# Kernel optimization log

Hardware: AMD Instinct MI355X
Metric: run time of the kernel (lower is better)

The kernel has to match this reference:

```python
import jax, jax.numpy as jnp
import numpy as np

N_SRC0, N_DST0 = 200000, 50000
N_DST1 = 10000
D_IN, D_HID = 128, 128


def _sage_mean(h, src, dst, n_dst, W_self, b_self, W_neigh, b_neigh, act):
    # gather messages from src nodes, mean-aggregate per dst node
    msg = h[src]                                             # [E, D]
    agg = jax.ops.segment_sum(msg, dst, num_segments=n_dst)  # [n_dst, D]
    deg = jax.ops.segment_sum(jnp.ones(dst.shape, h.dtype), dst, num_segments=n_dst)
    h_neigh = agg / jnp.maximum(deg, 1.0)[:, None]
    # DGL block convention: dst nodes are the first n_dst src nodes
    rst = h[:n_dst] @ W_self + b_self + h_neigh @ W_neigh + b_neigh
    return jax.nn.relu(rst) if act else rst


def setup_inputs() -> dict:
    key = jax.random.key(0)
    ks = jax.random.split(key, 12)
    s = 1.0 / np.sqrt(D_HID)
    return {
        "features": jax.random.normal(ks[0], (N_SRC0, D_IN), jnp.float32),
        "src0": jax.random.randint(ks[1], (800000,), 0, N_SRC0),
        "dst0": jax.random.randint(ks[2], (800000,), 0, N_DST0),
        "src1": jax.random.randint(ks[3], (160000,), 0, N_DST0),
        "dst1": jax.random.randint(ks[4], (160000,), 0, N_DST1),
        "W_init": jax.random.uniform(ks[5], (D_IN, D_HID), jnp.float32, -s, s),
        "b_init": jax.random.uniform(ks[6], (D_HID,), jnp.float32, -s, s),
        "W_self": jax.random.uniform(ks[7], (D_HID, D_HID), jnp.float32, -s, s),
        "b_self": jax.random.uniform(ks[8], (D_HID,), jnp.float32, -s, s),
        "W_neigh": jax.random.uniform(ks[9], (D_HID, D_HID), jnp.float32, -s, s),
        "b_neigh": jax.random.uniform(ks[10], (D_HID,), jnp.float32, -s, s),
    }


def reference(features, src0, dst0, src1, dst1, W_init, b_init, W_self, b_self, W_neigh, b_neigh):
    # fc_init + activation
    h = jax.nn.relu(features @ W_init + b_init)              # [N_SRC0, D_HID]
    # block 0 (act_flag True), dropout p=0.0 is identity
    h = _sage_mean(h, src0, dst0, N_DST0, W_self, b_self, W_neigh, b_neigh, act=True)
    # block 1 (last block: act_flag False)
    h = _sage_mean(h, src1, dst1, N_DST1, W_self, b_self, W_neigh, b_neigh, act=False)
    return jnp.squeeze(h, axis=1) if h.shape[1] == 1 else h  # h.squeeze(1) no-op for D_HID>1
```

## Files before the change

kernel.cpp:

```cpp
#include <hip/hip_runtime.h>
#include <stdint.h>
#include <stddef.h>


#define DIM 128
constexpr int N_SRC0 = 200000;
constexpr int N_DST0 = 50000;
constexpr int N_DST1 = 10000;
constexpr int E0 = 800000;
constexpr int E1 = 160000;
constexpr int MAXDEG = 64;

constexpr int FC_BLOCKS = 1024;
constexpr int PLACE_BLOCKS = 1024;
constexpr int PREP_BLOCKS = 16;

typedef __attribute__((ext_vector_type(8))) short bf16x8;
typedef __attribute__((ext_vector_type(4))) float f32x4;

__device__ __forceinline__ uint16_t f2bf(float f) {
  union { float f; uint32_t u; } v; v.f = f;
  return (uint16_t)((v.u + 0x7FFFu + ((v.u >> 16) & 1u)) >> 16);
}
__device__ __forceinline__ float bf2f(uint16_t h) {
  union { uint32_t u; float f; } v; v.u = ((uint32_t)h) << 16;
  return v.f;
}

__global__ __launch_bounds__(256, 4) void place_fc_kernel(
    const int* __restrict__ src0, const int* __restrict__ dst0,
    const int* __restrict__ src1, const int* __restrict__ dst1,
    int* __restrict__ cnt0, int* __restrict__ cnt1,
    int* __restrict__ eslot0, int* __restrict__ eslot1,
    const float* __restrict__ feat, const float* __restrict__ W_init,
    const float* __restrict__ bias, uint16_t* __restrict__ hout,
    const float* __restrict__ WS_src, const float* __restrict__ WN_src,
    uint16_t* __restrict__ Wf_out) {
  __shared__ __align__(16) float tile[2][4096];

  if (blockIdx.x >= PLACE_BLOCKS + FC_BLOCKS) {
    int pid = (blockIdx.x - (PLACE_BLOCKS + FC_BLOCKS)) * 256 + threadIdx.x;
#pragma unroll
    for (int u = 0; u < 8; u++) {
      int gid = pid * 8 + u;
      int m = gid >> 14, idx = gid & 16383;
      const float* W = m ? WN_src : WS_src;
      int j = idx & 7, lane = (idx >> 3) & 63, nt = (idx >> 9) & 7, kc = idx >> 12;
      int k = kc * 32 + (lane >> 4) * 8 + j;
      int n = nt * 16 + (lane & 15);
      Wf_out[gid] = f2bf(W[k * DIM + n]);
    }
    return;
  }

  if ((blockIdx.x & 1) == 0) {
    int pb = blockIdx.x >> 1;
    int part = pb & 7;
    int bpp  = PLACE_BLOCKS >> 3;
    int bidx = pb >> 3;
    const int4* s04 = (const int4*)src0;
    const int4* d04 = (const int4*)dst0;
    const int4* s14 = (const int4*)src1;
    const int4* d14 = (const int4*)dst1;

    int lo = part * (N_DST0 / 8), hi = lo + (N_DST0 / 8);
    for (int i = bidx * 256 + threadIdx.x; i < E0 / 4; i += bpp * 256) {
      int4 d = d04[i]; int4 s = s04[i];
      if (d.x >= lo && d.x < hi) { int p = atomicAdd(&cnt0[d.x], 1); if (p < MAXDEG) eslot0[(size_t)d.x * MAXDEG + p] = s.x; }
      if (d.y >= lo && d.y < hi) { int p = atomicAdd(&cnt0[d.y], 1); if (p < MAXDEG) eslot0[(size_t)d.y * MAXDEG + p] = s.y; }
      if (d.z >= lo && d.z < hi) { int p = atomicAdd(&cnt0[d.z], 1); if (p < MAXDEG) eslot0[(size_t)d.z * MAXDEG + p] = s.z; }
      if (d.w >= lo && d.w < hi) { int p = atomicAdd(&cnt0[d.w], 1); if (p < MAXDEG) eslot0[(size_t)d.w * MAXDEG + p] = s.w; }
    }
    int lo1 = part * (N_DST1 / 8), hi1 = lo1 + (N_DST1 / 8);
    for (int i = bidx * 256 + threadIdx.x; i < E1 / 4; i += bpp * 256) {
      int4 d = d14[i]; int4 s = s14[i];
      if (d.x >= lo1 && d.x < hi1) { int p = atomicAdd(&cnt1[d.x], 1); if (p < MAXDEG) eslot1[(size_t)d.x * MAXDEG + p] = s.x; }
      if (d.y >= lo1 && d.y < hi1) { int p = atomicAdd(&cnt1[d.y], 1); if (p < MAXDEG) eslot1[(size_t)d.y * MAXDEG + p] = s.y; }
      if (d.z >= lo1 && d.z < hi1) { int p = atomicAdd(&cnt1[d.z], 1); if (p < MAXDEG) eslot1[(size_t)d.z * MAXDEG + p] = s.z; }
      if (d.w >= lo1 && d.w < hi1) { int p = atomicAdd(&cnt1[d.w], 1); if (p < MAXDEG) eslot1[(size_t)d.w * MAXDEG + p] = s.w; }
    }
    return;
  }

  const int tid = threadIdx.x;
  const int w = tid >> 6, lane = tid & 63;
  const int q = lane >> 4, m16 = lane & 15;
  const int sl = w >> 1, nh = w & 1;

  {
    uint16_t* wtmp = (uint16_t*)tile;
    for (int u = 0; u < 8; u++) {
      int c = u * 256 + tid;
      int lane_c = c & 63;
      int nt = (c >> 6) & 7;
      int kc = c >> 9;
      int k0 = kc * 32 + (lane_c >> 4) * 8;
      int n  = nt * 16 + (lane_c & 15);
      bf16x8 frag;
#pragma unroll
      for (int j = 0; j < 8; j++)
        frag[j] = (short)f2bf(W_init[(size_t)(k0 + j) * DIM + n]);
      *(bf16x8*)&wtmp[(size_t)c * 8] = frag;
    }
  }
  __syncthreads();

  bf16x8 wv[4][4];
  {
    const uint16_t* wtmp = (const uint16_t*)tile;
#pragma unroll
    for (int kc = 0; kc < 4; kc++)
#pragma unroll
      for (int jj = 0; jj < 4; jj++)
        wv[kc][jj] = *(const bf16x8*)&wtmp[((kc * 8 + nh * 4 + jj) * 64 + lane) * 8];
  }
  __syncthreads();

  float bv[4];
#pragma unroll
  for (int j = 0; j < 4; j++) bv[j] = bias[(nh * 4 + j) * 16 + m16];

  const int ntiles = N_SRC0 / 32;

  const int lrow0 = w * 8 + (lane >> 5);
  auto stage = [&](int t, int buf) {
#pragma unroll
    for (int i = 0; i < 4; i++) {
      int row = lrow0 + i * 2;
      int g = (lane & 31) ^ (row & 7);
      const float* gs = feat + (size_t)t * 4096 + row * 128 + g * 4;
      float* ld = &tile[buf][w * 1024 + i * 256];
      __builtin_amdgcn_global_load_lds(
          (const __attribute__((address_space(1))) uint32_t*)gs,
          (__attribute__((address_space(3))) uint32_t*)ld,
          16, 0, 0);
    }
  };

  int t = blockIdx.x >> 1;
  int cur = 0;
  if (t < ntiles) stage(t, 0);

  const int trow = sl * 16 + m16;
  const int sw = trow & 7;

  while (t < ntiles) {
    int tn = t + FC_BLOCKS;
    if (tn < ntiles) {
      stage(tn, cur ^ 1);
      asm volatile("s_waitcnt vmcnt(4)" ::: "memory");
    } else {
      asm volatile("s_waitcnt vmcnt(0)" ::: "memory");
    }
    __builtin_amdgcn_s_barrier();
    __builtin_amdgcn_sched_barrier(0);

    f32x4 acc[4];
#pragma unroll
    for (int j = 0; j < 4; j++) acc[j] = (f32x4){0.f, 0.f, 0.f, 0.f};

    const char* rb = (const char*)&tile[cur][0] + trow * 512;
#pragma unroll
    for (int kc = 0; kc < 4; kc++) {
      int g0 = kc * 8 + q * 2;
      float4 x0 = *(const float4*)(rb + ((g0    ) ^ sw) * 16);
      float4 x1 = *(const float4*)(rb + ((g0 + 1) ^ sw) * 16);
      bf16x8 a;
      a[0] = (short)f2bf(x0.x); a[1] = (short)f2bf(x0.y);
      a[2] = (short)f2bf(x0.z); a[3] = (short)f2bf(x0.w);
      a[4] = (short)f2bf(x1.x); a[5] = (short)f2bf(x1.y);
      a[6] = (short)f2bf(x1.z); a[7] = (short)f2bf(x1.w);
#pragma unroll
      for (int j = 0; j < 4; j++)
        acc[j] = __builtin_amdgcn_mfma_f32_16x16x32_bf16(a, wv[kc][j], acc[j], 0, 0, 0);
    }

    int rowb = t * 32 + sl * 16 + q * 4;
#pragma unroll
    for (int j = 0; j < 4; j++)
#pragma unroll
      for (int r = 0; r < 4; r++) {
        float v = fmaxf(acc[j][r] + bv[j], 0.f);
        hout[(size_t)(rowb + r) * DIM + (nh * 4 + j) * 16 + m16] = f2bf(v);
      }

    __builtin_amdgcn_s_barrier();
    cur ^= 1;
    t = tn;
  }
}

template <bool ACT, bool OUT_BF16>
__global__ __launch_bounds__(256) void aggsage_kernel(
    const int* __restrict__ eslot, const int* __restrict__ deg,
    const uint16_t* __restrict__ hgat, const uint16_t* __restrict__ hself,
    const uint16_t* __restrict__ WfS, const uint16_t* __restrict__ WfN,
    const float* __restrict__ bS, const float* __restrict__ bN,
    void* __restrict__ outp) {
  __shared__ __align__(16) uint16_t hn_tile[16 * 128];

  const int strip = blockIdx.x;
  const int tid = threadIdx.x;
  const int w = tid >> 6, lane = tid & 63;
  const int qr = lane >> 4, c = lane & 15;

  for (int rr = 0; rr < 4; rr++) {
    int r = w + rr * 4;
    int d = strip * 16 + r;
    const int* sl = eslot + (size_t)d * MAXDEG;
    int dg = deg[d];
    int dgc = dg < MAXDEG ? dg : MAXDEG;

    float a0 = 0.f, a1 = 0.f, a2 = 0.f, a3 = 0.f;
    float a4 = 0.f, a5 = 0.f, a6 = 0.f, a7 = 0.f;

#define ACC4(P)                                                          \
    a0 += bf2f((uint16_t)(P).x); a1 += bf2f((uint16_t)((P).x >> 16));    \
    a2 += bf2f((uint16_t)(P).y); a3 += bf2f((uint16_t)((P).y >> 16));    \
    a4 += bf2f((uint16_t)(P).z); a5 += bf2f((uint16_t)((P).z >> 16));    \
    a6 += bf2f((uint16_t)(P).w); a7 += bf2f((uint16_t)((P).w >> 16));

    int e = 0;
    for (; e + 16 <= dgc; e += 16) {
      int s0 = sl[e + qr];
      int s1 = sl[e + 4 + qr];
      int s2 = sl[e + 8 + qr];
      int s3 = sl[e + 12 + qr];
      uint4 p0 = *(const uint4*)(hgat + (size_t)s0 * DIM + c * 8);
      uint4 p1 = *(const uint4*)(hgat + (size_t)s1 * DIM + c * 8);
      uint4 p2 = *(const uint4*)(hgat + (size_t)s2 * DIM + c * 8);
      uint4 p3 = *(const uint4*)(hgat + (size_t)s3 * DIM + c * 8);
      ACC4(p0); ACC4(p1); ACC4(p2); ACC4(p3);
    }
    for (; e + 8 <= dgc; e += 8) {
      int s0 = sl[e + qr];
      int s1 = sl[e + 4 + qr];
      uint4 p0 = *(const uint4*)(hgat + (size_t)s0 * DIM + c * 8);
      uint4 p1 = *(const uint4*)(hgat + (size_t)s1 * DIM + c * 8);
      ACC4(p0); ACC4(p1);
    }
    for (; e + 4 <= dgc; e += 4) {
      int s0 = sl[e + qr];
      uint4 p0 = *(const uint4*)(hgat + (size_t)s0 * DIM + c * 8);
      ACC4(p0);
    }
    int rem = dgc - e;
    if (qr < rem) {
      int s0 = sl[e + qr];
      uint4 p0 = *(const uint4*)(hgat + (size_t)s0 * DIM + c * 8);
      ACC4(p0);
    }
#undef ACC4

    a0 += __shfl_xor(a0, 16); a0 += __shfl_xor(a0, 32);
    a1 += __shfl_xor(a1, 16); a1 += __shfl_xor(a1, 32);
    a2 += __shfl_xor(a2, 16); a2 += __shfl_xor(a2, 32);
    a3 += __shfl_xor(a3, 16); a3 += __shfl_xor(a3, 32);
    a4 += __shfl_xor(a4, 16); a4 += __shfl_xor(a4, 32);
    a5 += __shfl_xor(a5, 16); a5 += __shfl_xor(a5, 32);
    a6 += __shfl_xor(a6, 16); a6 += __shfl_xor(a6, 32);
    a7 += __shfl_xor(a7, 16); a7 += __shfl_xor(a7, 32);

    if (qr == 0) {
      float inv = 1.f / fmaxf((float)dg, 1.f);
      uint4 o;
      o.x = (uint32_t)f2bf(a0 * inv) | ((uint32_t)f2bf(a1 * inv) << 16);
      o.y = (uint32_t)f2bf(a2 * inv) | ((uint32_t)f2bf(a3 * inv) << 16);
      o.z = (uint32_t)f2bf(a4 * inv) | ((uint32_t)f2bf(a5 * inv) << 16);
      o.w = (uint32_t)f2bf(a6 * inv) | ((uint32_t)f2bf(a7 * inv) << 16);
      int g = c ^ (r & 7);
      *(uint4*)&hn_tile[r * 128 + g * 8] = o;
    }
  }
  __syncthreads();

  const int q = lane >> 4, m16 = lane & 15;
  const int nt0 = w * 2;

  float bv[2];
#pragma unroll
  for (int j = 0; j < 2; j++)
    bv[j] = bS[(nt0 + j) * 16 + m16] + bN[(nt0 + j) * 16 + m16];

  bf16x8 XS[4], XN[4];
  {
    size_t ro = (size_t)(strip * 16 + m16) * DIM + q * 8;
#pragma unroll
    for (int kc = 0; kc < 4; kc++) {
      XS[kc] = *(const bf16x8*)(hself + ro + kc * 32);
      int g = (q + kc * 4) ^ (m16 & 7);
      XN[kc] = *(const bf16x8*)&hn_tile[m16 * 128 + g * 8];
    }
  }

  f32x4 acc[2];
#pragma unroll
  for (int j = 0; j < 2; j++) acc[j] = (f32x4){0.f, 0.f, 0.f, 0.f};

#pragma unroll
  for (int kc = 0; kc < 4; kc++)
#pragma unroll
    for (int j = 0; j < 2; j++) {
      size_t fo = (size_t)((kc * 8 + nt0 + j) * 64 + lane) * 8;
      bf16x8 ws = *(const bf16x8*)&WfS[fo];
      bf16x8 wn = *(const bf16x8*)&WfN[fo];
      acc[j] = __builtin_amdgcn_mfma_f32_16x16x32_bf16(XS[kc], ws, acc[j], 0, 0, 0);
      acc[j] = __builtin_amdgcn_mfma_f32_16x16x32_bf16(XN[kc], wn, acc[j], 0, 0, 0);
    }

  int m0 = strip * 16;
#pragma unroll
  for (int j = 0; j < 2; j++)
#pragma unroll
    for (int r = 0; r < 4; r++) {
      float v = acc[j][r] + bv[j];
      if (ACT) v = fmaxf(v, 0.f);
      size_t o = (size_t)(m0 + q * 4 + r) * DIM + (nt0 + j) * 16 + m16;
      if (OUT_BF16) ((uint16_t*)outp)[o] = f2bf(v);
      else          ((float*)outp)[o] = v;
    }
}

extern "C" void kernel_launch(void* const* d_in, const int* in_sizes, int n_in,
                              void* d_out, int out_size, void* d_ws, size_t ws_size,
                              hipStream_t stream) {
  const float* feat   = (const float*)d_in[0];
  const int* src0     = (const int*)d_in[1];
  const int* dst0     = (const int*)d_in[2];
  const int* src1     = (const int*)d_in[3];
  const int* dst1     = (const int*)d_in[4];
  const float* W_init = (const float*)d_in[5];
  const float* b_init = (const float*)d_in[6];
  const float* W_self = (const float*)d_in[7];
  const float* b_self = (const float*)d_in[8];
  const float* W_neigh= (const float*)d_in[9];
  const float* b_neigh= (const float*)d_in[10];

  char* ws = (char*)d_ws;
  uint16_t* h     = (uint16_t*)(ws + 0);
  uint16_t* h1    = (uint16_t*)(ws + 51200000);
  int*      cnt0  = (int*)(ws + 76800000);
  int*      cnt1  = (int*)(ws + 77000000);
  int*      eslot0= (int*)(ws + 77040000);
  int*      eslot1= (int*)(ws + 89840000);
  uint16_t* WfI   = (uint16_t*)(ws + 92400000);
  uint16_t* WfS   = WfI + 16384;
  uint16_t* WfN   = WfS + 16384;

  hipMemsetAsync(ws + 76800000, 0, 240000, stream);

  place_fc_kernel<<<PLACE_BLOCKS + FC_BLOCKS + PREP_BLOCKS, 256, 0, stream>>>(
      src0, dst0, src1, dst1, cnt0, cnt1, eslot0, eslot1,
      feat, W_init, b_init, h, W_self, W_neigh, WfS);

  aggsage_kernel<true, true><<<N_DST0 / 16, 256, 0, stream>>>(
      eslot0, cnt0, h, h, WfS, WfN, b_self, b_neigh, h1);

  aggsage_kernel<false, false><<<N_DST1 / 16, 256, 0, stream>>>(
      eslot1, cnt1, h1, h1, WfS, WfN, b_self, b_neigh, d_out);
}
```

Before: 277.4 us.

## Shrink FC tile to 16 rows per block to raise occupancy

The fused fc_init GEMM now processes 16-row tiles instead of 32. Each of the four waves owns two 16-column output slices instead of four, which halves the LDS double buffer and the per-thread weight registers. The launch bound hint rises from 4 to 6 blocks per SM to exploit the smaller footprint. The trade-off is twice as many loop iterations per block, each doing less work, plus more barriers and a staged two-pass weight load.

Measured after the change: 286.6 us. +3.3%, slower.

```diff
diff --git a/kernel.cpp b/kernel.cpp
--- a/kernel.cpp
+++ b/kernel.cpp
@@ -27,7 +27,7 @@
   return v.f;
 }
 
-__global__ __launch_bounds__(256, 4) void place_fc_kernel(
+__global__ __launch_bounds__(256, 6) void place_fc_kernel(
     const int* __restrict__ src0, const int* __restrict__ dst0,
     const int* __restrict__ src1, const int* __restrict__ dst1,
     int* __restrict__ cnt0, int* __restrict__ cnt1,
@@ -36,7 +36,7 @@
     const float* __restrict__ bias, uint16_t* __restrict__ hout,
     const float* __restrict__ WS_src, const float* __restrict__ WN_src,
     uint16_t* __restrict__ Wf_out) {
-  __shared__ __align__(16) float tile[2][4096];
+  __shared__ __align__(16) float tile[2][2048];
 
   if (blockIdx.x >= PLACE_BLOCKS + FC_BLOCKS) {
     int pid = (blockIdx.x - (PLACE_BLOCKS + FC_BLOCKS)) * 256 + threadIdx.x;
@@ -85,51 +85,51 @@
   const int tid = threadIdx.x;
   const int w = tid >> 6, lane = tid & 63;
   const int q = lane >> 4, m16 = lane & 15;
-  const int sl = w >> 1, nh = w & 1;
-
+
+  bf16x8 wv[4][2];
   {
     uint16_t* wtmp = (uint16_t*)tile;
-    for (int u = 0; u < 8; u++) {
-      int c = u * 256 + tid;
-      int lane_c = c & 63;
-      int nt = (c >> 6) & 7;
-      int kc = c >> 9;
-      int k0 = kc * 32 + (lane_c >> 4) * 8;
-      int n  = nt * 16 + (lane_c & 15);
-      bf16x8 frag;
-#pragma unroll
-      for (int j = 0; j < 8; j++)
-        frag[j] = (short)f2bf(W_init[(size_t)(k0 + j) * DIM + n]);
-      *(bf16x8*)&wtmp[(size_t)c * 8] = frag;
-    }
-  }
-  __syncthreads();
-
-  bf16x8 wv[4][4];
-  {
-    const uint16_t* wtmp = (const uint16_t*)tile;
-#pragma unroll
-    for (int kc = 0; kc < 4; kc++)
-#pragma unroll
-      for (int jj = 0; jj < 4; jj++)
-        wv[kc][jj] = *(const bf16x8*)&wtmp[((kc * 8 + nh * 4 + jj) * 64 + lane) * 8];
-  }
-  __syncthreads();
-
-  float bv[4];
-#pragma unroll
-  for (int j = 0; j < 4; j++) bv[j] = bias[(nh * 4 + j) * 16 + m16];
-
-  const int ntiles = N_SRC0 / 32;
-
-  const int lrow0 = w * 8 + (lane >> 5);
+#pragma unroll
+    for (int half = 0; half < 2; half++) {
+      for (int u = 0; u < 4; u++) {
+        int c = half * 1024 + u * 256 + tid;
+        int lane_c = c & 63;
+        int nt = (c >> 6) & 7;
+        int kc = c >> 9;
+        int k0 = kc * 32 + (lane_c >> 4) * 8;
+        int n  = nt * 16 + (lane_c & 15);
+        bf16x8 frag;
+#pragma unroll
+        for (int j = 0; j < 8; j++)
+          frag[j] = (short)f2bf(W_init[(size_t)(k0 + j) * DIM + n]);
+        *(bf16x8*)&wtmp[(size_t)(c - half * 1024) * 8] = frag;
+      }
+      __syncthreads();
+#pragma unroll
+      for (int kc2 = 0; kc2 < 2; kc2++) {
+        int kc = half * 2 + kc2;
+#pragma unroll
+        for (int jj = 0; jj < 2; jj++)
+          wv[kc][jj] = *(const bf16x8*)&wtmp[((kc2 * 8 + w * 2 + jj) * 64 + lane) * 8];
+      }
+      __syncthreads();
+    }
+  }
+
+  float bv[2];
+#pragma unroll
+  for (int j = 0; j < 2; j++) bv[j] = bias[(w * 2 + j) * 16 + m16];
+
+  const int ntiles = N_SRC0 / 16;
+
   auto stage = [&](int t, int buf) {
 #pragma unroll
-    for (int i = 0; i < 4; i++) {
-      int row = lrow0 + i * 2;
-      int g = (lane & 31) ^ (row & 7);
-      const float* gs = feat + (size_t)t * 4096 + row * 128 + g * 4;
-      float* ld = &tile[buf][w * 1024 + i * 256];
+    for (int i = 0; i < 2; i++) {
+      int gl = i * 256 + w * 64 + lane;
+      int row = gl >> 5;
+      int g = (gl & 31) ^ (row & 7);
+      const float* gs = feat + (size_t)t * 2048 + row * 128 + g * 4;
+      float* ld = &tile[buf][w * 256 + i * 1024];
       __builtin_amdgcn_global_load_lds(
           (const __attribute__((address_space(1))) uint32_t*)gs,
           (__attribute__((address_space(3))) uint32_t*)ld,
@@ -141,25 +141,24 @@
   int cur = 0;
   if (t < ntiles) stage(t, 0);
 
-  const int trow = sl * 16 + m16;
-  const int sw = trow & 7;
+  const int sw = m16 & 7;
 
   while (t < ntiles) {
     int tn = t + FC_BLOCKS;
     if (tn < ntiles) {
       stage(tn, cur ^ 1);
-      asm volatile("s_waitcnt vmcnt(4)" ::: "memory");
+      asm volatile("s_waitcnt vmcnt(2)" ::: "memory");
     } else {
       asm volatile("s_waitcnt vmcnt(0)" ::: "memory");
     }
     __builtin_amdgcn_s_barrier();
     __builtin_amdgcn_sched_barrier(0);
 
-    f32x4 acc[4];
-#pragma unroll
-    for (int j = 0; j < 4; j++) acc[j] = (f32x4){0.f, 0.f, 0.f, 0.f};
-
-    const char* rb = (const char*)&tile[cur][0] + trow * 512;
+    f32x4 acc[2];
+#pragma unroll
+    for (int j = 0; j < 2; j++) acc[j] = (f32x4){0.f, 0.f, 0.f, 0.f};
+
+    const char* rb = (const char*)&tile[cur][0] + m16 * 512;
 #pragma unroll
     for (int kc = 0; kc < 4; kc++) {
       int g0 = kc * 8 + q * 2;
@@ -171,17 +170,17 @@
       a[4] = (short)f2bf(x1.x); a[5] = (short)f2bf(x1.y);
       a[6] = (short)f2bf(x1.z); a[7] = (short)f2bf(x1.w);
 #pragma unroll
-      for (int j = 0; j < 4; j++)
+      for (int j = 0; j < 2; j++)
         acc[j] = __builtin_amdgcn_mfma_f32_16x16x32_bf16(a, wv[kc][j], acc[j], 0, 0, 0);
     }
 
-    int rowb = t * 32 + sl * 16 + q * 4;
-#pragma unroll
-    for (int j = 0; j < 4; j++)
+    int rowb = t * 16 + q * 4;
+#pragma unroll
+    for (int j = 0; j < 2; j++)
 #pragma unroll
       for (int r = 0; r < 4; r++) {
         float v = fmaxf(acc[j][r] + bv[j], 0.f);
-        hout[(size_t)(rowb + r) * DIM + (nh * 4 + j) * 16 + m16] = f2bf(v);
+        hout[(size_t)(rowb + r) * DIM + (w * 2 + j) * 16 + m16] = f2bf(v);
       }
 
     __builtin_amdgcn_s_barrier();
```
